# Kernel optimization log

Measured on AMD Instinct MI355X. Metric: run time of the kernel, lower is better.

## Reference

```python
import jax, jax.numpy as jnp
import numpy as np

B, H, S, D = 4, 16, 2048, 64

def setup_inputs() -> dict:
    key = jax.random.key(0)
    kq, kk, kv = jax.random.split(key, 3)
    q = jax.random.normal(kq, (B, H, S, D), dtype=jnp.float32)
    k = jax.random.normal(kk, (B, H, S, D), dtype=jnp.float32)
    v = jax.random.normal(kv, (B, H, S, D), dtype=jnp.float32)
    return {"q": q, "k": k, "v": v}

def reference(q, k, v):
    # dots: [b,h,i,j] = q . k (NO 1/sqrt(d) scaling, matching source)
    dots = jnp.einsum('bhid,bhjd->bhij', q, k)
    # causal=False (and the source's causal mask is a no-op bug anyway)
    attn = jax.nn.softmax(dots, axis=-1)
    # out: [b,h,i,d] = sum_j attn[b,h,i,j] * v[b,h,j,d]
    return jnp.einsum('bhjd,bhij->bhid', v, attn)
```

## Files before the change

### kernel.cpp

```cpp
#include <hip/hip_runtime.h>
#include <hip/hip_bf16.h>
#include <stdint.h>

#define B_ 4
#define H_ 16
#define S_ 2048
#define D_ 64
#define QBLK 128
#define KBLK 64
#define LDW 72

typedef __attribute__((ext_vector_type(8))) short short8;
typedef __attribute__((ext_vector_type(4))) float f32x4;
typedef __attribute__((ext_vector_type(16))) float f32x16;
typedef _Float16 f16x8 __attribute__((ext_vector_type(8)));
typedef _Float16 f16x4 __attribute__((ext_vector_type(4)));
typedef __fp16 fp16x2 __attribute__((ext_vector_type(2)));

__device__ __forceinline__ unsigned short f2bf(float f) {
  union { float f; unsigned int u; } x; x.f = f;
  unsigned int u = x.u;
  unsigned int r = (u + 0x7FFFu + ((u >> 16) & 1u)) >> 16;
  return (unsigned short)r;
}
__device__ __forceinline__ float bf2f(unsigned short h) {
  union { unsigned int u; float f; } y; y.u = ((unsigned int)h) << 16;
  return y.f;
}

__device__ __forceinline__ unsigned pkrtz(float a, float b) {
  union { fp16x2 h; unsigned u; } c;
  c.h = __builtin_amdgcn_cvt_pkrtz(a, b);
  return c.u;
}

__device__ __forceinline__ void swap32(unsigned &a, unsigned &b) {
#if __has_builtin(__builtin_amdgcn_permlane32_swap)
  typedef int i32x2 __attribute__((ext_vector_type(2)));
  i32x2 r = __builtin_amdgcn_permlane32_swap((int)a, (int)b, false, false);
  a = (unsigned)r[0]; b = (unsigned)r[1];
#else
  unsigned pa = (unsigned)__shfl_xor((int)a, 32);
  unsigned pb = (unsigned)__shfl_xor((int)b, 32);
  bool lo = (threadIdx.x & 32) == 0;
  unsigned r0 = lo ? a : pb;
  unsigned r1 = lo ? pa : b;
  a = r0; b = r1;
#endif
}

#define GLOAD16(g, l) __builtin_amdgcn_global_load_lds( \
    (const __attribute__((address_space(1))) unsigned int*)(g), \
    (__attribute__((address_space(3))) unsigned int*)(l), 16, 0, 0)

__global__ void prep_k(const float* __restrict__ K, _Float16* __restrict__ Kp) {
  int e4 = (blockIdx.x * 256 + threadIdx.x) * 4;
  int bh  = e4 >> 17;
  int rem = e4 & 131071;
  int s   = rem >> 6;
  int d0  = rem & 63;
  const float4 kv = *(const float4*)(K + (size_t)e4);
  f16x4 h;
  h[0] = (_Float16)kv.x; h[1] = (_Float16)kv.y;
  h[2] = (_Float16)kv.z; h[3] = (_Float16)kv.w;
  size_t off = ((size_t)bh * S_ + s) * 128 + (unsigned)((d0 * 2) ^ ((s & 7) << 4));
  *(f16x4*)((char*)Kp + off) = h;
}

__global__ void prep_v(const float* __restrict__ V, _Float16* __restrict__ Vt) {
  __shared__ _Float16 tile[64][68];
  int bh = blockIdx.x >> 5;
  int st = blockIdx.x & 31;
  const float* Vb = V + ((size_t)bh * S_ + st * 64) * 64;
  int tid = threadIdx.x;
  #pragma unroll
  for (int i = 0; i < 4; ++i) {
    int idx = i * 1024 + tid * 4;
    int r = idx >> 6, c = idx & 63;
    float4 vv = *(const float4*)(Vb + (size_t)r * 64 + c);
    f16x4 o;
    o[0] = (_Float16)vv.x; o[1] = (_Float16)vv.y;
    o[2] = (_Float16)vv.z; o[3] = (_Float16)vv.w;
    *(f16x4*)&tile[r][c] = o;
  }
  __syncthreads();
  int chunk = tid & 15;
  int dbase = tid >> 4;
  size_t outb = (size_t)bh * (64 * S_ * 2) + (size_t)st * 128;
  #pragma unroll
  for (int i = 0; i < 4; ++i) {
    int d = dbase + i * 16;
    f16x4 o;
    o[0] = tile[chunk * 4 + 0][d];
    o[1] = tile[chunk * 4 + 1][d];
    o[2] = tile[chunk * 4 + 2][d];
    o[3] = tile[chunk * 4 + 3][d];
    size_t off = outb + (size_t)d * (S_ * 2) + (unsigned)((chunk * 8) ^ ((d & 7) << 4));
    *(f16x4*)((char*)Vt + off) = o;
  }
}

__global__ __launch_bounds__(256)
void attn_fwd4(const float* __restrict__ Q, const _Float16* __restrict__ Kg,
               const _Float16* __restrict__ Vg, float* __restrict__ O) {
  __shared__ char smem[32768];

  const int tid  = threadIdx.x;
  const int lane = tid & 63;
  const int wid  = tid >> 6;
  const int l31  = lane & 31;
  const int hi   = lane >> 5;

  const int qtile = blockIdx.x;
  const int bh    = blockIdx.y;

  const char* KB = (const char*)Kg + (size_t)bh * (S_ * 128);
  const char* VB = (const char*)Vg + (size_t)bh * (64 * S_ * 2);
  const float* Qb = Q + (size_t)bh * S_ * D_;
  float*       Ob = O + (size_t)bh * S_ * D_;

  const int qrow = qtile * QBLK + wid * 32 + l31;
  f16x8 qf[4];
  #pragma unroll
  for (int ds = 0; ds < 4; ++ds) {
    const float* qp = Qb + (size_t)qrow * D_ + ds * 16 + hi * 8;
    float4 a = *(const float4*)(qp);
    float4 b = *(const float4*)(qp + 4);
    qf[ds][0] = (_Float16)a.x; qf[ds][1] = (_Float16)a.y;
    qf[ds][2] = (_Float16)a.z; qf[ds][3] = (_Float16)a.w;
    qf[ds][4] = (_Float16)b.x; qf[ds][5] = (_Float16)b.y;
    qf[ds][6] = (_Float16)b.z; qf[ds][7] = (_Float16)b.w;
  }

  f32x16 oacc[2];
  #pragma unroll
  for (int dn = 0; dn < 2; ++dn)
    #pragma unroll
    for (int r = 0; r < 16; ++r) oacc[dn][r] = 0.f;
  float m_r = -INFINITY, l_r = 0.f;

  #define STAGE(buf, kb)                                                        \
    {                                                                           \
      char* Kl_ = smem + (buf) * 16384;                                         \
      char* Vl_ = Kl_ + 8192;                                                   \
      _Pragma("unroll")                                                         \
      for (int c = 0; c < 4; ++c) {                                             \
        int id = c * 4 + wid;                                                   \
        if (id < 8) {                                                           \
          GLOAD16(KB + (size_t)(kb) * 128 + id * 1024 + lane * 16,              \
                  Kl_ + id * 1024);                                             \
        } else {                                                                \
          int i = id - 8;                                                       \
          GLOAD16(VB + (size_t)(i * 8 + (lane >> 3)) * (S_ * 2)                 \
                     + ((kb) >> 6) * 128 + (lane & 7) * 16,                     \
                  Vl_ + i * 1024);                                              \
        }                                                                       \
      }                                                                         \
    }

  STAGE(0, 0);
  __syncthreads();

  for (int it = 0; it < S_ / KBLK; ++it) {
    const int cur = it & 1;
    if (it < S_ / KBLK - 1) STAGE(cur ^ 1, (it + 1) * KBLK);

    const char* Kl = smem + cur * 16384;
    const char* Vl = Kl + 8192;

    f32x16 sacc[2];
    #pragma unroll
    for (int b = 0; b < 2; ++b) {
      #pragma unroll
      for (int r = 0; r < 16; ++r) sacc[b][r] = 0.f;
      const int row = b * 32 + l31;
      #pragma unroll
      for (int ds = 0; ds < 4; ++ds) {
        f16x8 kf = *(const f16x8*)(Kl + row * 128 + ((ds * 32 + hi * 16) ^ ((row & 7) << 4)));
        sacc[b] = __builtin_amdgcn_mfma_f32_32x32x16_f16(kf, qf[ds], sacc[b], 0, 0, 0);
      }
    }

    float t[16];
    #pragma unroll
    for (int r = 0; r < 16; ++r) t[r] = fmaxf(sacc[0][r], sacc[1][r]);
    #pragma unroll
    for (int s = 8; s > 0; s >>= 1)
      #pragma unroll
      for (int r = 0; r < 8; ++r)
        if (r < s) t[r] = fmaxf(t[r], t[r + s]);
    float mx = fmaxf(t[0], __shfl_xor(t[0], 32));
    float nm = fmaxf(m_r, mx);
    float sc = __expf(m_r - nm);
    m_r = nm;

    float rs0 = 0.f, rs1 = 0.f;
    #pragma unroll
    for (int b = 0; b < 2; ++b)
      #pragma unroll
      for (int r = 0; r < 16; ++r) {
        float p = __expf(sacc[b][r] - nm);
        sacc[b][r] = p;
        if (r & 1) rs1 += p; else rs0 += p;
      }
    float rs = rs0 + rs1;
    rs += __shfl_xor(rs, 32);
    l_r = l_r * sc + rs;
    #pragma unroll
    for (int dn = 0; dn < 2; ++dn)
      #pragma unroll
      for (int r = 0; r < 16; ++r) oacc[dn][r] *= sc;

    unsigned ww[2][8];
    #pragma unroll
    for (int b = 0; b < 2; ++b)
      #pragma unroll
      for (int r1 = 0; r1 < 4; ++r1) {
        ww[b][r1 * 2 + 0] = pkrtz(sacc[b][4 * r1 + 0], sacc[b][4 * r1 + 1]);
        ww[b][r1 * 2 + 1] = pkrtz(sacc[b][4 * r1 + 2], sacc[b][4 * r1 + 3]);
      }

    f16x8 pb[4];
    #pragma unroll
    for (int ks = 0; ks < 4; ++ks) {
      const int b = ks >> 1, e = (ks & 1) * 2;
      unsigned u0 = ww[b][e * 2 + 0];
      unsigned u1 = ww[b][e * 2 + 1];
      unsigned u2 = ww[b][(e + 1) * 2 + 0];
      unsigned u3 = ww[b][(e + 1) * 2 + 1];
      swap32(u0, u2);
      swap32(u1, u3);
      union { unsigned u[4]; f16x8 v; } c;
      c.u[0] = u0; c.u[1] = u1; c.u[2] = u2; c.u[3] = u3;
      pb[ks] = c.v;
    }

    #pragma unroll
    for (int dn = 0; dn < 2; ++dn) {
      const int d = dn * 32 + l31;
      #pragma unroll
      for (int ks = 0; ks < 4; ++ks) {
        f16x8 vf = *(const f16x8*)(Vl + d * 128 + ((ks * 32 + hi * 16) ^ ((d & 7) << 4)));
        oacc[dn] = __builtin_amdgcn_mfma_f32_32x32x16_f16(vf, pb[ks], oacc[dn], 0, 0, 0);
      }
    }
    __syncthreads();
  }
  #undef STAGE

  const float inv = 1.0f / l_r;
  float* Ep = (float*)(smem + wid * 8192);
  #pragma unroll
  for (int dn = 0; dn < 2; ++dn)
    #pragma unroll
    for (int r = 0; r < 16; ++r) {
      int d = dn * 32 + (r & 3) + 8 * (r >> 2) + 4 * hi;
      Ep[d * 32 + l31] = oacc[dn][r] * inv;
    }
  __syncthreads();
  const int q2 = lane >> 1, dh = lane & 1;
  float* orow = Ob + (size_t)(qtile * QBLK + wid * 32 + q2) * D_ + dh * 32;
  #pragma unroll
  for (int c = 0; c < 8; ++c) {
    float4 o4;
    o4.x = Ep[(dh * 32 + c * 4 + 0) * 32 + q2];
    o4.y = Ep[(dh * 32 + c * 4 + 1) * 32 + q2];
    o4.z = Ep[(dh * 32 + c * 4 + 2) * 32 + q2];
    o4.w = Ep[(dh * 32 + c * 4 + 3) * 32 + q2];
    *(float4*)(orow + c * 4) = o4;
  }
}

__global__ __launch_bounds__(256, 2)
void attn_fwd(const float* __restrict__ Q, const float* __restrict__ K,
              const float* __restrict__ V, float* __restrict__ O) {
  __shared__ alignas(16) unsigned short Kh_lds[KBLK * LDW];
  __shared__ alignas(16) unsigned short Kl_lds[KBLK * LDW];
  __shared__ alignas(16) unsigned short Vt_lds[D_ * LDW];
  __shared__ alignas(16) unsigned short P_lds[4][16 * LDW];

  const int tid  = threadIdx.x;
  const int lane = tid & 63;
  const int wid  = tid >> 6;
  const int l15  = lane & 15;
  const int dgrp = lane >> 4;

  const int qtile = blockIdx.x;
  const int bh    = blockIdx.y;

  const size_t base = (size_t)bh * S_ * D_;
  const float* Qb = Q + base;
  const float* Kb = K + base;
  const float* Vb = V + base;
  float*       Ob = O + base;

  const int qrow = qtile * 64 + wid * 16 + l15;
  short8 qfh[2], qfl[2];
  {
    const float* qp = Qb + (size_t)qrow * D_ + dgrp * 8;
    #pragma unroll
    for (int s = 0; s < 2; ++s)
      #pragma unroll
      for (int j = 0; j < 8; ++j) {
        float f = qp[s * 32 + j];
        unsigned short h = f2bf(f);
        qfh[s][j] = (short)h;
        qfl[s][j] = (short)f2bf(f - bf2f(h));
      }
  }

  f32x4 oacc[4];
  #pragma unroll
  for (int t = 0; t < 4; ++t) oacc[t] = f32x4{0.f, 0.f, 0.f, 0.f};
  float m_r[4], l_r[4];
  #pragma unroll
  for (int j = 0; j < 4; ++j) { m_r[j] = -INFINITY; l_r[j] = 0.f; }

  for (int kb = 0; kb < S_; kb += KBLK) {
    __syncthreads();
    #pragma unroll
    for (int c = 0; c < 4; ++c) {
      int e = (c * 256 + tid) * 4;
      int r = e >> 6, col = e & 63;
      const float4 kv = *(const float4*)(Kb + (size_t)(kb + r) * D_ + col);
      ushort4 kh, kl;
      kh.x = f2bf(kv.x); kl.x = f2bf(kv.x - bf2f(kh.x));
      kh.y = f2bf(kv.y); kl.y = f2bf(kv.y - bf2f(kh.y));
      kh.z = f2bf(kv.z); kl.z = f2bf(kv.z - bf2f(kh.z));
      kh.w = f2bf(kv.w); kl.w = f2bf(kv.w - bf2f(kh.w));
      *(ushort4*)&Kh_lds[r * LDW + col] = kh;
      *(ushort4*)&Kl_lds[r * LDW + col] = kl;
      const float4 vv = *(const float4*)(Vb + (size_t)(kb + r) * D_ + col);
      Vt_lds[(col + 0) * LDW + r] = f2bf(vv.x);
      Vt_lds[(col + 1) * LDW + r] = f2bf(vv.y);
      Vt_lds[(col + 2) * LDW + r] = f2bf(vv.z);
      Vt_lds[(col + 3) * LDW + r] = f2bf(vv.w);
    }
    __syncthreads();

    f32x4 sa[4];
    #pragma unroll
    for (int t = 0; t < 4; ++t) {
      sa[t] = f32x4{0.f, 0.f, 0.f, 0.f};
      #pragma unroll
      for (int s = 0; s < 2; ++s) {
        const int off = (t * 16 + l15) * LDW + s * 32 + dgrp * 8;
        short8 kfh = *(const short8*)&Kh_lds[off];
        short8 kfl = *(const short8*)&Kl_lds[off];
        sa[t] = __builtin_amdgcn_mfma_f32_16x16x32_bf16(qfh[s], kfh, sa[t], 0, 0, 0);
        sa[t] = __builtin_amdgcn_mfma_f32_16x16x32_bf16(qfh[s], kfl, sa[t], 0, 0, 0);
        sa[t] = __builtin_amdgcn_mfma_f32_16x16x32_bf16(qfl[s], kfh, sa[t], 0, 0, 0);
      }
    }

    float pmax[4];
    #pragma unroll
    for (int j = 0; j < 4; ++j) {
      float mx = fmaxf(fmaxf(sa[0][j], sa[1][j]), fmaxf(sa[2][j], sa[3][j]));
      #pragma unroll
      for (int m = 1; m < 16; m <<= 1) mx = fmaxf(mx, __shfl_xor(mx, m));
      pmax[j] = mx;
    }
    float scale[4];
    #pragma unroll
    for (int j = 0; j < 4; ++j) {
      float nm = fmaxf(m_r[j], pmax[j]);
      scale[j] = __expf(m_r[j] - nm);
      m_r[j] = nm;
    }
    float rs[4] = {0.f, 0.f, 0.f, 0.f};
    #pragma unroll
    for (int t = 0; t < 4; ++t)
      #pragma unroll
      for (int j = 0; j < 4; ++j) {
        float p = __expf(sa[t][j] - m_r[j]);
        rs[j] += p;
        P_lds[wid][(dgrp * 4 + j) * LDW + t * 16 + l15] = f2bf(p);
      }
    #pragma unroll
    for (int j = 0; j < 4; ++j) {
      #pragma unroll
      for (int m = 1; m < 16; m <<= 1) rs[j] += __shfl_xor(rs[j], m);
      l_r[j] = l_r[j] * scale[j] + rs[j];
      #pragma unroll
      for (int t = 0; t < 4; ++t) oacc[t][j] *= scale[j];
    }

    #pragma unroll
    for (int s = 0; s < 2; ++s) {
      short8 pf = *(const short8*)&P_lds[wid][l15 * LDW + s * 32 + dgrp * 8];
      #pragma unroll
      for (int t = 0; t < 4; ++t) {
        short8 vf = *(const short8*)&Vt_lds[(t * 16 + l15) * LDW + s * 32 + dgrp * 8];
        oacc[t] = __builtin_amdgcn_mfma_f32_16x16x32_bf16(pf, vf, oacc[t], 0, 0, 0);
      }
    }
  }

  #pragma unroll
  for (int j = 0; j < 4; ++j) {
    float inv = 1.0f / l_r[j];
    int row = qtile * 64 + wid * 16 + dgrp * 4 + j;
    float* op = Ob + (size_t)row * D_ + l15;
    #pragma unroll
    for (int t = 0; t < 4; ++t)
      op[t * 16] = oacc[t][j] * inv;
  }
}

extern "C" void kernel_launch(void* const* d_in, const int* in_sizes, int n_in,
                              void* d_out, int out_size, void* d_ws, size_t ws_size,
                              hipStream_t stream) {
  const float* q = (const float*)d_in[0];
  const float* k = (const float*)d_in[1];
  const float* v = (const float*)d_in[2];
  float* o = (float*)d_out;
  const size_t PLANE = (size_t)B_ * H_ * S_ * 128;
  if (ws_size >= 2 * PLANE) {
    _Float16* Kp = (_Float16*)d_ws;
    _Float16* Vt = (_Float16*)((char*)d_ws + PLANE);
    prep_k<<<8192, 256, 0, stream>>>(k, Kp);
    prep_v<<<2048, 256, 0, stream>>>(v, Vt);
    attn_fwd4<<<dim3(S_ / QBLK, B_ * H_), 256, 0, stream>>>(q, Kp, Vt, o);
  } else {
    attn_fwd<<<dim3(S_ / 64, B_ * H_), 256, 0, stream>>>(q, k, v, o);
  }
}
```

Measured before the change: 151.1 us.

## Use exp2 softmax with lazy rescaling, fdot2 row sums and MFMA priority hints

Q is prescaled by log2(e) so the softmax uses native exp2 instead of exp. The running max and output rescale are updated only when some lane's new max exceeds the old by more than 8, which skips the per-iteration oacc multiply. Row sums are computed from the packed fp16 probabilities via fdot2, the max reduction uses a shallower tree with permlane swap, and setprio is raised around the MFMA blocks. The trade-off is probabilities up to 256 stored in fp16 and row sums taken from rounded values.

```diff
diff --git a/kernel.cpp b/kernel.cpp
--- a/kernel.cpp
+++ b/kernel.cpp
@@ -9,6 +9,7 @@
 #define QBLK 128
 #define KBLK 64
 #define LDW 72
+#define LOG2E 1.44269504088896340736f
 
 typedef __attribute__((ext_vector_type(8))) short short8;
 typedef __attribute__((ext_vector_type(4))) float f32x4;
@@ -32,6 +33,17 @@
   union { fp16x2 h; unsigned u; } c;
   c.h = __builtin_amdgcn_cvt_pkrtz(a, b);
   return c.u;
+}
+__device__ __forceinline__ fp16x2 u2h(unsigned u) {
+  union { unsigned u; fp16x2 h; } c; c.u = u; return c.h;
+}
+
+__device__ __forceinline__ float fast_exp2(float x) {
+#if __has_builtin(__builtin_amdgcn_exp2f)
+  return __builtin_amdgcn_exp2f(x);
+#else
+  return exp2f(x);
+#endif
 }
 
 __device__ __forceinline__ void swap32(unsigned &a, unsigned &b) {
@@ -49,6 +61,17 @@
 #endif
 }
 
+__device__ __forceinline__ float pairmax(float x) {
+  unsigned a = __float_as_uint(x), b = a;
+  swap32(a, b);
+  return fmaxf(__uint_as_float(a), __uint_as_float(b));
+}
+__device__ __forceinline__ float pairsum(float x) {
+  unsigned a = __float_as_uint(x), b = a;
+  swap32(a, b);
+  return __uint_as_float(a) + __uint_as_float(b);
+}
+
 #define GLOAD16(g, l) __builtin_amdgcn_global_load_lds( \
     (const __attribute__((address_space(1))) unsigned int*)(g), \
     (__attribute__((address_space(3))) unsigned int*)(l), 16, 0, 0)
@@ -126,10 +149,10 @@
     const float* qp = Qb + (size_t)qrow * D_ + ds * 16 + hi * 8;
     float4 a = *(const float4*)(qp);
     float4 b = *(const float4*)(qp + 4);
-    qf[ds][0] = (_Float16)a.x; qf[ds][1] = (_Float16)a.y;
-    qf[ds][2] = (_Float16)a.z; qf[ds][3] = (_Float16)a.w;
-    qf[ds][4] = (_Float16)b.x; qf[ds][5] = (_Float16)b.y;
-    qf[ds][6] = (_Float16)b.z; qf[ds][7] = (_Float16)b.w;
+    qf[ds][0] = (_Float16)(a.x * LOG2E); qf[ds][1] = (_Float16)(a.y * LOG2E);
+    qf[ds][2] = (_Float16)(a.z * LOG2E); qf[ds][3] = (_Float16)(a.w * LOG2E);
+    qf[ds][4] = (_Float16)(b.x * LOG2E); qf[ds][5] = (_Float16)(b.y * LOG2E);
+    qf[ds][6] = (_Float16)(b.z * LOG2E); qf[ds][7] = (_Float16)(b.w * LOG2E);
   }
 
   f32x16 oacc[2];
@@ -169,6 +192,7 @@
     const char* Vl = Kl + 8192;
 
     f32x16 sacc[2];
+    __builtin_amdgcn_s_setprio(1);
     #pragma unroll
     for (int b = 0; b < 2; ++b) {
       #pragma unroll
@@ -180,45 +204,72 @@
         sacc[b] = __builtin_amdgcn_mfma_f32_32x32x16_f16(kf, qf[ds], sacc[b], 0, 0, 0);
       }
     }
-
-    float t[16];
-    #pragma unroll
-    for (int r = 0; r < 16; ++r) t[r] = fmaxf(sacc[0][r], sacc[1][r]);
-    #pragma unroll
-    for (int s = 8; s > 0; s >>= 1)
-      #pragma unroll
-      for (int r = 0; r < 8; ++r)
-        if (r < s) t[r] = fmaxf(t[r], t[r + s]);
-    float mx = fmaxf(t[0], __shfl_xor(t[0], 32));
-    float nm = fmaxf(m_r, mx);
-    float sc = __expf(m_r - nm);
-    m_r = nm;
-
+    __builtin_amdgcn_s_setprio(0);
+
+    float u[16];
+    #pragma unroll
+    for (int r = 0; r < 16; ++r) u[r] = fmaxf(sacc[0][r], sacc[1][r]);
+    float w0 = fmaxf(fmaxf(u[0], u[1]), u[2]);
+    float w1 = fmaxf(fmaxf(u[3], u[4]), u[5]);
+    float w2 = fmaxf(fmaxf(u[6], u[7]), u[8]);
+    float w3 = fmaxf(fmaxf(u[9], u[10]), u[11]);
+    float w4 = fmaxf(fmaxf(u[12], u[13]), u[14]);
+    float x0 = fmaxf(fmaxf(w0, w1), w2);
+    float x1 = fmaxf(fmaxf(w3, w4), u[15]);
+    float mx = pairmax(fmaxf(x0, x1));
+
+    if (!__all(mx <= m_r + 8.f)) {
+      float nm = fmaxf(m_r, mx);
+      float sc = fast_exp2(m_r - nm);
+      m_r = nm;
+      l_r *= sc;
+      #pragma unroll
+      for (int dn = 0; dn < 2; ++dn)
+        #pragma unroll
+        for (int r = 0; r < 16; ++r) oacc[dn][r] *= sc;
+    }
+
+    unsigned ww[2][8];
+#if !__has_builtin(__builtin_amdgcn_fdot2)
     float rs0 = 0.f, rs1 = 0.f;
+#endif
     #pragma unroll
     for (int b = 0; b < 2; ++b)
       #pragma unroll
-      for (int r = 0; r < 16; ++r) {
-        float p = __expf(sacc[b][r] - nm);
-        sacc[b][r] = p;
-        if (r & 1) rs1 += p; else rs0 += p;
-      }
-    float rs = rs0 + rs1;
-    rs += __shfl_xor(rs, 32);
-    l_r = l_r * sc + rs;
-    #pragma unroll
-    for (int dn = 0; dn < 2; ++dn)
-      #pragma unroll
-      for (int r = 0; r < 16; ++r) oacc[dn][r] *= sc;
-
-    unsigned ww[2][8];
-    #pragma unroll
-    for (int b = 0; b < 2; ++b)
-      #pragma unroll
       for (int r1 = 0; r1 < 4; ++r1) {
-        ww[b][r1 * 2 + 0] = pkrtz(sacc[b][4 * r1 + 0], sacc[b][4 * r1 + 1]);
-        ww[b][r1 * 2 + 1] = pkrtz(sacc[b][4 * r1 + 2], sacc[b][4 * r1 + 3]);
-      }
+        float p0 = fast_exp2(sacc[b][4 * r1 + 0] - m_r);
+        float p1 = fast_exp2(sacc[b][4 * r1 + 1] - m_r);
+        float p2 = fast_exp2(sacc[b][4 * r1 + 2] - m_r);
+        float p3 = fast_exp2(sacc[b][4 * r1 + 3] - m_r);
+        ww[b][r1 * 2 + 0] = pkrtz(p0, p1);
+        ww[b][r1 * 2 + 1] = pkrtz(p2, p3);
+#if !__has_builtin(__builtin_amdgcn_fdot2)
+        rs0 += p0 + p2; rs1 += p1 + p3;
+#endif
+      }
+
+    float rs;
+#if __has_builtin(__builtin_amdgcn_fdot2)
+    {
+      const fp16x2 ones = {(__fp16)1.f, (__fp16)1.f};
+      float rA = 0.f, rB = 0.f, rC = 0.f, rD = 0.f;
+      #pragma unroll
+      for (int b = 0; b < 2; ++b) {
+        rA = __builtin_amdgcn_fdot2(u2h(ww[b][0]), ones, rA, false);
+        rB = __builtin_amdgcn_fdot2(u2h(ww[b][1]), ones, rB, false);
+        rC = __builtin_amdgcn_fdot2(u2h(ww[b][2]), ones, rC, false);
+        rD = __builtin_amdgcn_fdot2(u2h(ww[b][3]), ones, rD, false);
+        rA = __builtin_amdgcn_fdot2(u2h(ww[b][4]), ones, rA, false);
+        rB = __builtin_amdgcn_fdot2(u2h(ww[b][5]), ones, rB, false);
+        rC = __builtin_amdgcn_fdot2(u2h(ww[b][6]), ones, rC, false);
+        rD = __builtin_amdgcn_fdot2(u2h(ww[b][7]), ones, rD, false);
+      }
+      rs = (rA + rB) + (rC + rD);
+    }
+#else
+    rs = rs0 + rs1;
+#endif
+    l_r += pairsum(rs);
 
     f16x8 pb[4];
     #pragma unroll
@@ -235,6 +286,7 @@
       pb[ks] = c.v;
     }
 
+    __builtin_amdgcn_s_setprio(1);
     #pragma unroll
     for (int dn = 0; dn < 2; ++dn) {
       const int d = dn * 32 + l31;
@@ -244,6 +296,7 @@
         oacc[dn] = __builtin_amdgcn_mfma_f32_32x32x16_f16(vf, pb[ks], oacc[dn], 0, 0, 0);
       }
     }
+    __builtin_amdgcn_s_setprio(0);
     __syncthreads();
   }
   #undef STAGE
```

After: 145.4 us. -3.7%, faster.
